# Kernel optimization log

Hardware: AMD Instinct MI355X
Metric: run time of the kernel (lower is better)

The kernel has to match this reference:

```python
import jax, jax.numpy as jnp
import numpy as np

NUM_Q = 4        # len(n_e_list)
N_E = 2048       # codes per quantizer level
E_DIM = 128      # e_dim
N_TOK = 32768    # flattened tokens
BETA = 0.25      # commitment coefficient


def setup_inputs() -> dict:
    key = jax.random.key(0)
    k_x, k_cb = jax.random.split(key)
    x = jax.random.normal(k_x, (N_TOK, E_DIM), dtype=jnp.float32)
    codebooks = jax.random.normal(k_cb, (NUM_Q, N_E, E_DIM), dtype=jnp.float32) * 0.1
    return {"x": x, "codebooks": codebooks, "use_freq": 0}


def _vq_layer(res, cb):
    # res: [N, D], cb: [K, D]
    # squared euclidean distance via expansion: ||r||^2 - 2 r.c + ||c||^2
    d = (jnp.sum(res * res, axis=-1, keepdims=True)
         - 2.0 * (res @ cb.T)
         + jnp.sum(cb * cb, axis=-1))            # [N, K]
    idx = jnp.argmin(d, axis=-1)                  # [N]
    q = cb[idx]                                   # [N, D] gather
    sg = jax.lax.stop_gradient
    # VQ-VAE loss: codebook term + beta * commitment term
    loss = jnp.mean((q - sg(res)) ** 2) + BETA * jnp.mean((sg(q) - res) ** 2)
    q_st = res + sg(q - res)                      # straight-through estimator
    return q_st, loss, idx


def reference(x, codebooks, use_freq):
    # residual chain over NUM_Q quantizer levels (sequential dependency)
    def step(carry, cb):
        residual, x_q = carry
        q, loss, idx = _vq_layer(residual, cb)
        return (residual - q, x_q + q), (loss, idx)

    (residual, x_q), (losses, indices) = jax.lax.scan(
        step, (x, jnp.zeros_like(x)), codebooks)
    mean_loss = jnp.mean(losses)
    all_indices = jnp.moveaxis(indices, 0, -1)    # [N, NUM_Q]
    return x_q, mean_loss, all_indices
```

## Files before the change

### kernel.cpp

```cpp
#include <hip/hip_runtime.h>

#define NTOK 32768
#define NE   2048
#define EDIM 128
#define NQ   4

#define TOKT 64
#define CHCODES 64
#define NCHUNK (NE / CHCODES)
#define CAP 16
#define MARGIN 0.25f

typedef __attribute__((ext_vector_type(8))) short short8v;
typedef __attribute__((ext_vector_type(4))) float f32x4;

__device__ __forceinline__ unsigned short bf16rne(float x) {
    unsigned u = __float_as_uint(x);
    unsigned r = 0x7FFFu + ((u >> 16) & 1u);
    return (unsigned short)((u + r) >> 16);
}

__device__ __forceinline__ void gld16(const void* g, const void* l) {
    __builtin_amdgcn_global_load_lds(
        (const __attribute__((address_space(1))) unsigned int*)g,
        (__attribute__((address_space(3))) unsigned int*)l, 16, 0, 0);
}

#define MFMA_BF16 __builtin_amdgcn_mfma_f32_16x16x32_bf16

__global__ __launch_bounds__(256) void prep_kernel(
    const float* __restrict__ cb, unsigned short* __restrict__ cb16s,
    float* __restrict__ cnorm, float* __restrict__ loss_accum)
{
    const int row = blockIdx.x * 256 + threadIdx.x;
    if (row == 0) *loss_accum = 0.0f;
    const float* src = cb + (size_t)row * EDIM;
    unsigned short* dst = cb16s + (size_t)row * EDIM;
    const int swz8 = (row & 7) << 3;
    float s = 0.0f;
#pragma unroll
    for (int j = 0; j < EDIM / 4; ++j) {
        float4 v = ((const float4*)src)[j];
        s += v.x * v.x; s += v.y * v.y; s += v.z * v.z; s += v.w * v.w;
        ushort4 o;
        o.x = bf16rne(v.x); o.y = bf16rne(v.y);
        o.z = bf16rne(v.z); o.w = bf16rne(v.w);
        *(ushort4*)(dst + ((j * 4) ^ swz8)) = o;
    }
    cnorm[row] = s;
}

__global__ __launch_bounds__(256, 2) void vq_level_kernel(
    const float* __restrict__ rin,
    const float* __restrict__ cbF,
    const unsigned short* __restrict__ cbL,
    const float* __restrict__ cnorm,
    float* __restrict__ rout,
    float* __restrict__ xq,
    float* __restrict__ idx_out,
    float* __restrict__ loss_accum,
    int level, int first)
{
    __shared__ __align__(16) float Af[TOKT][132];
    __shared__ __align__(16) unsigned short Bs[2][CHCODES * EDIM];
    __shared__ float part[4 * TOKT];
    __shared__ float rns[TOKT];
    __shared__ float mdw[2][TOKT];
    __shared__ int   cnt[TOKT];
    __shared__ int   lst[TOKT * CAP];
    __shared__ float redb_d[4][TOKT];
    __shared__ int   redb_i[4][TOKT];
    __shared__ int   idx_s[TOKT];
    __shared__ float lsum[256];

    const int t     = threadIdx.x;
    const int tok0  = blockIdx.x * TOKT;
    const int w     = t >> 6;
    const int rh    = w >> 1;
    const int chalf = w & 1;
    const int cl    = t & 15;
    const int lg    = (t & 63) >> 4;
    if (t < TOKT) cnt[t] = 0;

    {
        const int tok = t & 63;
        const int dg  = t >> 6;
        float s = 0.0f;
#pragma unroll
        for (int j = 0; j < 8; ++j) {
            const int d0 = dg * 32 + j * 4;
            float4 v = *(const float4*)(rin + (size_t)(tok0 + tok) * EDIM + d0);
            *(float4*)&Af[tok][d0] = v;
            s += v.x * v.x; s += v.y * v.y; s += v.z * v.z; s += v.w * v.w;
        }
        part[dg * TOKT + tok] = s;
    }
    __syncthreads();
    if (t < TOKT)
        rns[t] = ((part[t] + part[TOKT + t]) + part[2 * TOKT + t])
                 + part[3 * TOKT + t];

    short8v a00, a01, a02, a03, a10, a11, a12, a13;
#define LDA(AF, AROW, KT) { \
    float4 p0 = *(const float4*)&Af[AROW][(KT) * 32 + lg * 8]; \
    float4 p1 = *(const float4*)&Af[AROW][(KT) * 32 + lg * 8 + 4]; \
    AF[0] = (short)bf16rne(p0.x); AF[1] = (short)bf16rne(p0.y); \
    AF[2] = (short)bf16rne(p0.z); AF[3] = (short)bf16rne(p0.w); \
    AF[4] = (short)bf16rne(p1.x); AF[5] = (short)bf16rne(p1.y); \
    AF[6] = (short)bf16rne(p1.z); AF[7] = (short)bf16rne(p1.w); }
    {
        const int ar0 = rh * 32 + cl, ar1 = rh * 32 + 16 + cl;
        LDA(a00, ar0, 0) LDA(a01, ar0, 1) LDA(a02, ar0, 2) LDA(a03, ar0, 3)
        LDA(a10, ar1, 0) LDA(a11, ar1, 1) LDA(a12, ar1, 2) LDA(a13, ar1, 3)
    }
#undef LDA

    const int swzk = (cl & 7) << 4;
    const int inn0 = (0   + lg * 16) ^ swzk;
    const int inn1 = (64  + lg * 16) ^ swzk;
    const int inn2 = (128 + lg * 16) ^ swzk;
    const int inn3 = (192 + lg * 16) ^ swzk;

#define STAGE(DST, CH) { \
    const char* gs = (const char*)cbL + (size_t)(CH) * 16384 + t * 16; \
    char* ls = (char*)(DST) + (t & 192) * 16; \
    gld16(gs,         ls); \
    gld16(gs + 4096,  ls + 4096); \
    gld16(gs + 8192,  ls + 8192); \
    gld16(gs + 12288, ls + 12288); }

#define MFMAG(BUFC, CH, CT, TAIL) { \
    const char* bp = (const char*)&Bs[BUFC][0] \
                     + (chalf * 32 + (CT) * 16 + cl) * 256; \
    short8v b0 = *(const short8v*)(bp + inn0); \
    short8v b1 = *(const short8v*)(bp + inn1); \
    short8v b2 = *(const short8v*)(bp + inn2); \
    short8v b3 = *(const short8v*)(bp + inn3); \
    f32x4 ac0 = {0.f, 0.f, 0.f, 0.f}; \
    f32x4 ac1 = {0.f, 0.f, 0.f, 0.f}; \
    ac0 = MFMA_BF16(a00, b0, ac0, 0, 0, 0); \
    ac0 = MFMA_BF16(a01, b1, ac0, 0, 0, 0); \
    ac0 = MFMA_BF16(a02, b2, ac0, 0, 0, 0); \
    ac0 = MFMA_BF16(a03, b3, ac0, 0, 0, 0); \
    ac1 = MFMA_BF16(a10, b0, ac1, 0, 0, 0); \
    ac1 = MFMA_BF16(a11, b1, ac1, 0, 0, 0); \
    ac1 = MFMA_BF16(a12, b2, ac1, 0, 0, 0); \
    ac1 = MFMA_BF16(a13, b3, ac1, 0, 0, 0); \
    const int code = (CH) * CHCODES + chalf * 32 + (CT) * 16 + cl; \
    const float cn = cnorm[code]; \
    TAIL }

#define T_MIN \
    md00 = fminf(md00, (rn00 - 2.f * ac0[0]) + cn); \
    md01 = fminf(md01, (rn01 - 2.f * ac0[1]) + cn); \
    md02 = fminf(md02, (rn02 - 2.f * ac0[2]) + cn); \
    md03 = fminf(md03, (rn03 - 2.f * ac0[3]) + cn); \
    md10 = fminf(md10, (rn10 - 2.f * ac1[0]) + cn); \
    md11 = fminf(md11, (rn11 - 2.f * ac1[1]) + cn); \
    md12 = fminf(md12, (rn12 - 2.f * ac1[2]) + cn); \
    md13 = fminf(md13, (rn13 - 2.f * ac1[3]) + cn);

#define PUSH(AC, R, RN, TH, TOKB) { \
    float dd = ((RN) - 2.f * AC[R]) + cn; \
    if (dd < (TH)) { int p = atomicAdd(&cnt[(TOKB) + R], 1); \
                     if (p < CAP) lst[((TOKB) + R) * CAP + p] = code; } }
#define T_CAND \
    PUSH(ac0, 0, rn00, th00, tokb0) PUSH(ac0, 1, rn01, th01, tokb0) \
    PUSH(ac0, 2, rn02, th02, tokb0) PUSH(ac0, 3, rn03, th03, tokb0) \
    PUSH(ac1, 0, rn10, th10, tokb1) PUSH(ac1, 1, rn11, th11, tokb1) \
    PUSH(ac1, 2, rn12, th12, tokb1) PUSH(ac1, 3, rn13, th13, tokb1)

#define CH_P1(B, CH) { MFMAG(B, CH, 0, T_MIN)  MFMAG(B, CH, 1, T_MIN)  }
#define CH_P2(B, CH) { MFMAG(B, CH, 0, T_CAND) MFMAG(B, CH, 1, T_CAND) }

    STAGE(&Bs[0][0], 0)
    __syncthreads();

    const int tokb0 = rh * 32 + lg * 4;
    const int tokb1 = tokb0 + 16;
    const float rn00 = rns[tokb0 + 0], rn01 = rns[tokb0 + 1];
    const float rn02 = rns[tokb0 + 2], rn03 = rns[tokb0 + 3];
    const float rn10 = rns[tokb1 + 0], rn11 = rns[tokb1 + 1];
    const float rn12 = rns[tokb1 + 2], rn13 = rns[tokb1 + 3];

    float md00 = 3.402823466e38f, md01 = md00, md02 = md00, md03 = md00;
    float md10 = md00, md11 = md00, md12 = md00, md13 = md00;

    for (int c2 = 0; c2 < NCHUNK / 2; ++c2) {
        const int c = c2 * 2;
        STAGE(&Bs[1][0], c + 1)
        CH_P1(0, c)
        __syncthreads();
        if (c + 2 < NCHUNK) STAGE(&Bs[0][0], c + 2)
        CH_P1(1, c + 1)
        __syncthreads();
    }

#pragma unroll
    for (int m = 1; m < 16; m <<= 1) {
        md00 = fminf(md00, __shfl_xor(md00, m, 64));
        md01 = fminf(md01, __shfl_xor(md01, m, 64));
        md02 = fminf(md02, __shfl_xor(md02, m, 64));
        md03 = fminf(md03, __shfl_xor(md03, m, 64));
        md10 = fminf(md10, __shfl_xor(md10, m, 64));
        md11 = fminf(md11, __shfl_xor(md11, m, 64));
        md12 = fminf(md12, __shfl_xor(md12, m, 64));
        md13 = fminf(md13, __shfl_xor(md13, m, 64));
    }
    if (cl == 0) {
        mdw[chalf][tokb0 + 0] = md00; mdw[chalf][tokb0 + 1] = md01;
        mdw[chalf][tokb0 + 2] = md02; mdw[chalf][tokb0 + 3] = md03;
        mdw[chalf][tokb1 + 0] = md10; mdw[chalf][tokb1 + 1] = md11;
        mdw[chalf][tokb1 + 2] = md12; mdw[chalf][tokb1 + 3] = md13;
    }

    STAGE(&Bs[0][0], 0)
    __syncthreads();

    const float th00 = fminf(mdw[0][tokb0 + 0], mdw[1][tokb0 + 0]) + MARGIN;
    const float th01 = fminf(mdw[0][tokb0 + 1], mdw[1][tokb0 + 1]) + MARGIN;
    const float th02 = fminf(mdw[0][tokb0 + 2], mdw[1][tokb0 + 2]) + MARGIN;
    const float th03 = fminf(mdw[0][tokb0 + 3], mdw[1][tokb0 + 3]) + MARGIN;
    const float th10 = fminf(mdw[0][tokb1 + 0], mdw[1][tokb1 + 0]) + MARGIN;
    const float th11 = fminf(mdw[0][tokb1 + 1], mdw[1][tokb1 + 1]) + MARGIN;
    const float th12 = fminf(mdw[0][tokb1 + 2], mdw[1][tokb1 + 2]) + MARGIN;
    const float th13 = fminf(mdw[0][tokb1 + 3], mdw[1][tokb1 + 3]) + MARGIN;

    for (int c2 = 0; c2 < NCHUNK / 2; ++c2) {
        const int c = c2 * 2;
        STAGE(&Bs[1][0], c + 1)
        CH_P2(0, c)
        __syncthreads();
        if (c + 2 < NCHUNK) STAGE(&Bs[0][0], c + 2)
        CH_P2(1, c + 1)
        __syncthreads();
    }

    {
        const int tok = t & 63;
        const int s   = t >> 6;
        const int n   = min(cnt[tok], CAP);
        const float rn_t = rns[tok];
        float bd = 3.402823466e38f;
        int   bi = 0x7fffffff;
        for (int i = s; i < n; i += 4) {
            const int c = lst[tok * CAP + i];
            const float* cr = cbF + (size_t)c * EDIM;
            float dot = 0.0f;
#pragma unroll 8
            for (int d = 0; d < EDIM; ++d)
                dot = fmaf(Af[tok][d], cr[d], dot);
            const float dd = (rn_t - 2.0f * dot) + cnorm[c];
            if (dd < bd || (dd == bd && c < bi)) { bd = dd; bi = c; }
        }
        redb_d[s][tok] = bd;
        redb_i[s][tok] = bi;
    }
    __syncthreads();
    if (t < TOKT) {
        float bd = redb_d[0][t];
        int   bi = redb_i[0][t];
#pragma unroll
        for (int s = 1; s < 4; ++s) {
            const float dd = redb_d[s][t];
            const int   ii = redb_i[s][t];
            if (dd < bd || (dd == bd && ii < bi)) { bd = dd; bi = ii; }
        }
        idx_s[t] = bi;
        idx_out[(size_t)(tok0 + t) * NQ + level] = (float)bi;
    }
    __syncthreads();

    {
        const int tok = t >> 2;
        const int dq  = t & 3;
        const int gi  = idx_s[tok];
        const float* qrow = cbF + (size_t)gi * EDIM;
        float lp = 0.0f;
#pragma unroll
        for (int k = 0; k < 8; ++k) {
            const int d0 = k * 16 + dq * 4;
            const float4 q = *(const float4*)(qrow + d0);
            const float4 r = *(const float4*)&Af[tok][d0];
            float4 tq, qst, rnv;
            tq.x = q.x - r.x; tq.y = q.y - r.y; tq.z = q.z - r.z; tq.w = q.w - r.w;
            qst.x = r.x + tq.x; qst.y = r.y + tq.y;
            qst.z = r.z + tq.z; qst.w = r.w + tq.w;
            rnv.x = r.x - qst.x; rnv.y = r.y - qst.y;
            rnv.z = r.z - qst.z; rnv.w = r.w - qst.w;
            const size_t go = (size_t)(tok0 + tok) * EDIM + d0;
            *(float4*)(rout + go) = rnv;
            if (first) {
                *(float4*)(xq + go) = qst;
            } else {
                float4 o = *(const float4*)(xq + go);
                o.x += qst.x; o.y += qst.y; o.z += qst.z; o.w += qst.w;
                *(float4*)(xq + go) = o;
            }
            lp += tq.x * tq.x; lp += tq.y * tq.y;
            lp += tq.z * tq.z; lp += tq.w * tq.w;
        }
        lsum[t] = lp;
    }
    __syncthreads();
#pragma unroll
    for (int s2 = 128; s2 > 0; s2 >>= 1) {
        if (t < s2) lsum[t] += lsum[t + s2];
        __syncthreads();
    }
    if (t == 0) atomicAdd(loss_accum, lsum[0]);
}

__global__ void finalize_kernel(const float* __restrict__ loss_accum,
                                float* __restrict__ out_loss)
{
    *out_loss = *loss_accum * (1.25f / (4.0f * (float)NTOK * (float)EDIM));
}

extern "C" void kernel_launch(void* const* d_in, const int* in_sizes, int n_in,
                              void* d_out, int out_size, void* d_ws, size_t ws_size,
                              hipStream_t stream)
{
    const float* x  = (const float*)d_in[0];
    const float* cb = (const float*)d_in[1];

    float* out      = (float*)d_out;
    float* xq       = out;
    float* out_loss = out + (size_t)NTOK * EDIM;
    float* idx_out  = out + (size_t)NTOK * EDIM + 1;

    float* ws             = (float*)d_ws;
    float* cnorm          = ws;
    float* loss_accum     = ws + 8192;
    unsigned short* cb16s = (unsigned short*)(ws + 8448);
    float* r0             = ws + 8448 + (size_t)NQ * NE * EDIM / 2;

    prep_kernel<<<(NQ * NE) / 256, 256, 0, stream>>>(cb, cb16s, cnorm, loss_accum);

    for (int l = 0; l < NQ; ++l) {
        const float* rin = (l == 0) ? x : r0;
        vq_level_kernel<<<NTOK / TOKT, 256, 0, stream>>>(
            rin, cb + (size_t)l * NE * EDIM,
            cb16s + (size_t)l * NE * EDIM,
            cnorm + (size_t)l * NE,
            r0, xq, idx_out, loss_accum, l, (l == 0) ? 1 : 0);
    }
    finalize_kernel<<<1, 1, 0, stream>>>(loss_accum, out_loss);
}
```

Baseline: 291.7 us.

## Replace two-pass bf16 argmin with single pass plus per-half-chunk max filtering

Removes the second full MFMA sweep over the codebook. A single pass now computes scores (dot minus half the code norm, folded into the accumulator init), keeps a per-token running max, and records a ceiling-encoded 16-bit max for each 32-code half-chunk in shared memory. Half-chunks whose max lies within a margin of the best are placed on a worklist and rescored exactly in fp32, with a packed 64-bit atomicMin picking the winner. This halves MFMA and LDS staging work and drops the per-code atomic candidate pushes, at the cost of rescoring 32 codes per surviving half-chunk, a worklist cap of 512 that can overflow and drop candidates, and shared buffers aliased onto the staging buffer.

```diff
diff --git a/kernel.cpp b/kernel.cpp
--- a/kernel.cpp
+++ b/kernel.cpp
@@ -8,8 +8,9 @@
 #define TOKT 64
 #define CHCODES 64
 #define NCHUNK (NE / CHCODES)
-#define CAP 16
-#define MARGIN 0.25f
+#define NHC 64
+#define WLCAP 512
+#define MARGIN_S 0.25f
 
 typedef __attribute__((ext_vector_type(8))) short short8v;
 typedef __attribute__((ext_vector_type(4))) float f32x4;
@@ -18,6 +19,14 @@
     unsigned u = __float_as_uint(x);
     unsigned r = 0x7FFFu + ((u >> 16) & 1u);
     return (unsigned short)((u + r) >> 16);
+}
+
+__device__ __forceinline__ unsigned enc32f(float f) {
+    unsigned u = __float_as_uint(f);
+    return u ^ ((unsigned)((int)u >> 31) | 0x80000000u);
+}
+__device__ __forceinline__ unsigned short enc16ceil(float f) {
+    return (unsigned short)((enc32f(f) >> 16) + 1);
 }
 
 __device__ __forceinline__ void gld16(const void* g, const void* l) {
@@ -63,15 +72,18 @@
 {
     __shared__ __align__(16) float Af[TOKT][132];
     __shared__ __align__(16) unsigned short Bs[2][CHCODES * EDIM];
-    __shared__ float part[4 * TOKT];
+    __shared__ unsigned short chm[TOKT * NHC];
     __shared__ float rns[TOKT];
-    __shared__ float mdw[2][TOKT];
-    __shared__ int   cnt[TOKT];
-    __shared__ int   lst[TOKT * CAP];
-    __shared__ float redb_d[4][TOKT];
-    __shared__ int   redb_i[4][TOKT];
-    __shared__ int   idx_s[TOKT];
-    __shared__ float lsum[256];
+
+    float* part = (float*)&Bs[1][0];
+    char*  ov   = (char*)&Bs[0][0];
+    unsigned long long* best = (unsigned long long*)ov;
+    int*   wl    = (int*)(ov + 512);
+    int*   wcnt  = (int*)(ov + 2560);
+    float* smaxs = (float*)(ov + 2576);
+    float* mdw   = (float*)(ov + 2832);
+    int*   idx_s = (int*)(ov + 3344);
+    float* lsum  = (float*)(ov + 3600);
 
     const int t     = threadIdx.x;
     const int tok0  = blockIdx.x * TOKT;
@@ -80,7 +92,6 @@
     const int chalf = w & 1;
     const int cl    = t & 15;
     const int lg    = (t & 63) >> 4;
-    if (t < TOKT) cnt[t] = 0;
 
     {
         const int tok = t & 63;
@@ -129,143 +140,171 @@
     gld16(gs + 8192,  ls + 8192); \
     gld16(gs + 12288, ls + 12288); }
 
-#define MFMAG(BUFC, CH, CT, TAIL) { \
-    const char* bp = (const char*)&Bs[BUFC][0] \
-                     + (chalf * 32 + (CT) * 16 + cl) * 256; \
-    short8v b0 = *(const short8v*)(bp + inn0); \
-    short8v b1 = *(const short8v*)(bp + inn1); \
-    short8v b2 = *(const short8v*)(bp + inn2); \
-    short8v b3 = *(const short8v*)(bp + inn3); \
-    f32x4 ac0 = {0.f, 0.f, 0.f, 0.f}; \
-    f32x4 ac1 = {0.f, 0.f, 0.f, 0.f}; \
-    ac0 = MFMA_BF16(a00, b0, ac0, 0, 0, 0); \
-    ac0 = MFMA_BF16(a01, b1, ac0, 0, 0, 0); \
-    ac0 = MFMA_BF16(a02, b2, ac0, 0, 0, 0); \
-    ac0 = MFMA_BF16(a03, b3, ac0, 0, 0, 0); \
-    ac1 = MFMA_BF16(a10, b0, ac1, 0, 0, 0); \
-    ac1 = MFMA_BF16(a11, b1, ac1, 0, 0, 0); \
-    ac1 = MFMA_BF16(a12, b2, ac1, 0, 0, 0); \
-    ac1 = MFMA_BF16(a13, b3, ac1, 0, 0, 0); \
-    const int code = (CH) * CHCODES + chalf * 32 + (CT) * 16 + cl; \
-    const float cn = cnorm[code]; \
-    TAIL }
-
-#define T_MIN \
-    md00 = fminf(md00, (rn00 - 2.f * ac0[0]) + cn); \
-    md01 = fminf(md01, (rn01 - 2.f * ac0[1]) + cn); \
-    md02 = fminf(md02, (rn02 - 2.f * ac0[2]) + cn); \
-    md03 = fminf(md03, (rn03 - 2.f * ac0[3]) + cn); \
-    md10 = fminf(md10, (rn10 - 2.f * ac1[0]) + cn); \
-    md11 = fminf(md11, (rn11 - 2.f * ac1[1]) + cn); \
-    md12 = fminf(md12, (rn12 - 2.f * ac1[2]) + cn); \
-    md13 = fminf(md13, (rn13 - 2.f * ac1[3]) + cn);
-
-#define PUSH(AC, R, RN, TH, TOKB) { \
-    float dd = ((RN) - 2.f * AC[R]) + cn; \
-    if (dd < (TH)) { int p = atomicAdd(&cnt[(TOKB) + R], 1); \
-                     if (p < CAP) lst[((TOKB) + R) * CAP + p] = code; } }
-#define T_CAND \
-    PUSH(ac0, 0, rn00, th00, tokb0) PUSH(ac0, 1, rn01, th01, tokb0) \
-    PUSH(ac0, 2, rn02, th02, tokb0) PUSH(ac0, 3, rn03, th03, tokb0) \
-    PUSH(ac1, 0, rn10, th10, tokb1) PUSH(ac1, 1, rn11, th11, tokb1) \
-    PUSH(ac1, 2, rn12, th12, tokb1) PUSH(ac1, 3, rn13, th13, tokb1)
-
-#define CH_P1(B, CH) { MFMAG(B, CH, 0, T_MIN)  MFMAG(B, CH, 1, T_MIN)  }
-#define CH_P2(B, CH) { MFMAG(B, CH, 0, T_CAND) MFMAG(B, CH, 1, T_CAND) }
-
-    STAGE(&Bs[0][0], 0)
-    __syncthreads();
-
     const int tokb0 = rh * 32 + lg * 4;
     const int tokb1 = tokb0 + 16;
-    const float rn00 = rns[tokb0 + 0], rn01 = rns[tokb0 + 1];
-    const float rn02 = rns[tokb0 + 2], rn03 = rns[tokb0 + 3];
-    const float rn10 = rns[tokb1 + 0], rn11 = rns[tokb1 + 1];
-    const float rn12 = rns[tokb1 + 2], rn13 = rns[tokb1 + 3];
-
-    float md00 = 3.402823466e38f, md01 = md00, md02 = md00, md03 = md00;
+
+#define CHUNK(BUFC, CH) { \
+    const char* bpA = (const char*)&Bs[BUFC][0] + (chalf * 32 + cl) * 256; \
+    const int codeA = (CH) * 64 + chalf * 32 + cl; \
+    const float cnA = -0.5f * cnorm[codeA]; \
+    const float cnB = -0.5f * cnorm[codeA + 16]; \
+    short8v b0 = *(const short8v*)(bpA + inn0); \
+    short8v b1 = *(const short8v*)(bpA + inn1); \
+    short8v b2 = *(const short8v*)(bpA + inn2); \
+    short8v b3 = *(const short8v*)(bpA + inn3); \
+    f32x4 p00 = {cnA, cnA, cnA, cnA}; \
+    f32x4 p01 = {cnA, cnA, cnA, cnA}; \
+    p00 = MFMA_BF16(a00, b0, p00, 0, 0, 0); \
+    p00 = MFMA_BF16(a01, b1, p00, 0, 0, 0); \
+    p00 = MFMA_BF16(a02, b2, p00, 0, 0, 0); \
+    p00 = MFMA_BF16(a03, b3, p00, 0, 0, 0); \
+    p01 = MFMA_BF16(a10, b0, p01, 0, 0, 0); \
+    p01 = MFMA_BF16(a11, b1, p01, 0, 0, 0); \
+    p01 = MFMA_BF16(a12, b2, p01, 0, 0, 0); \
+    p01 = MFMA_BF16(a13, b3, p01, 0, 0, 0); \
+    const char* bpB = bpA + 16 * 256; \
+    b0 = *(const short8v*)(bpB + inn0); \
+    b1 = *(const short8v*)(bpB + inn1); \
+    b2 = *(const short8v*)(bpB + inn2); \
+    b3 = *(const short8v*)(bpB + inn3); \
+    f32x4 p10 = {cnB, cnB, cnB, cnB}; \
+    f32x4 p11 = {cnB, cnB, cnB, cnB}; \
+    p10 = MFMA_BF16(a00, b0, p10, 0, 0, 0); \
+    p10 = MFMA_BF16(a01, b1, p10, 0, 0, 0); \
+    p10 = MFMA_BF16(a02, b2, p10, 0, 0, 0); \
+    p10 = MFMA_BF16(a03, b3, p10, 0, 0, 0); \
+    p11 = MFMA_BF16(a10, b0, p11, 0, 0, 0); \
+    p11 = MFMA_BF16(a11, b1, p11, 0, 0, 0); \
+    p11 = MFMA_BF16(a12, b2, p11, 0, 0, 0); \
+    p11 = MFMA_BF16(a13, b3, p11, 0, 0, 0); \
+    float lm0 = fmaxf(p00[0], p10[0]); md00 = fmaxf(md00, lm0); \
+    float lm1 = fmaxf(p00[1], p10[1]); md01 = fmaxf(md01, lm1); \
+    float lm2 = fmaxf(p00[2], p10[2]); md02 = fmaxf(md02, lm2); \
+    float lm3 = fmaxf(p00[3], p10[3]); md03 = fmaxf(md03, lm3); \
+    float lm4 = fmaxf(p01[0], p11[0]); md10 = fmaxf(md10, lm4); \
+    float lm5 = fmaxf(p01[1], p11[1]); md11 = fmaxf(md11, lm5); \
+    float lm6 = fmaxf(p01[2], p11[2]); md12 = fmaxf(md12, lm6); \
+    float lm7 = fmaxf(p01[3], p11[3]); md13 = fmaxf(md13, lm7); \
+    _Pragma("unroll") \
+    for (int m = 1; m < 16; m <<= 1) { \
+        lm0 = fmaxf(lm0, __shfl_xor(lm0, m, 64)); \
+        lm1 = fmaxf(lm1, __shfl_xor(lm1, m, 64)); \
+        lm2 = fmaxf(lm2, __shfl_xor(lm2, m, 64)); \
+        lm3 = fmaxf(lm3, __shfl_xor(lm3, m, 64)); \
+        lm4 = fmaxf(lm4, __shfl_xor(lm4, m, 64)); \
+        lm5 = fmaxf(lm5, __shfl_xor(lm5, m, 64)); \
+        lm6 = fmaxf(lm6, __shfl_xor(lm6, m, 64)); \
+        lm7 = fmaxf(lm7, __shfl_xor(lm7, m, 64)); \
+    } \
+    if (cl == 0) { \
+        const int hc = (CH) * 2 + chalf; \
+        chm[(tokb0 + 0) * NHC + hc] = enc16ceil(lm0); \
+        chm[(tokb0 + 1) * NHC + hc] = enc16ceil(lm1); \
+        chm[(tokb0 + 2) * NHC + hc] = enc16ceil(lm2); \
+        chm[(tokb0 + 3) * NHC + hc] = enc16ceil(lm3); \
+        chm[(tokb1 + 0) * NHC + hc] = enc16ceil(lm4); \
+        chm[(tokb1 + 1) * NHC + hc] = enc16ceil(lm5); \
+        chm[(tokb1 + 2) * NHC + hc] = enc16ceil(lm6); \
+        chm[(tokb1 + 3) * NHC + hc] = enc16ceil(lm7); \
+    } }
+
+    STAGE(&Bs[0][0], 0)
+    __syncthreads();
+
+    float md00 = -3.402823466e38f, md01 = md00, md02 = md00, md03 = md00;
     float md10 = md00, md11 = md00, md12 = md00, md13 = md00;
 
     for (int c2 = 0; c2 < NCHUNK / 2; ++c2) {
         const int c = c2 * 2;
         STAGE(&Bs[1][0], c + 1)
-        CH_P1(0, c)
+        CHUNK(0, c)
         __syncthreads();
         if (c + 2 < NCHUNK) STAGE(&Bs[0][0], c + 2)
-        CH_P1(1, c + 1)
+        CHUNK(1, c + 1)
         __syncthreads();
     }
+#undef CHUNK
 
 #pragma unroll
     for (int m = 1; m < 16; m <<= 1) {
-        md00 = fminf(md00, __shfl_xor(md00, m, 64));
-        md01 = fminf(md01, __shfl_xor(md01, m, 64));
-        md02 = fminf(md02, __shfl_xor(md02, m, 64));
-        md03 = fminf(md03, __shfl_xor(md03, m, 64));
-        md10 = fminf(md10, __shfl_xor(md10, m, 64));
-        md11 = fminf(md11, __shfl_xor(md11, m, 64));
-        md12 = fminf(md12, __shfl_xor(md12, m, 64));
-        md13 = fminf(md13, __shfl_xor(md13, m, 64));
+        md00 = fmaxf(md00, __shfl_xor(md00, m, 64));
+        md01 = fmaxf(md01, __shfl_xor(md01, m, 64));
+        md02 = fmaxf(md02, __shfl_xor(md02, m, 64));
+        md03 = fmaxf(md03, __shfl_xor(md03, m, 64));
+        md10 = fmaxf(md10, __shfl_xor(md10, m, 64));
+        md11 = fmaxf(md11, __shfl_xor(md11, m, 64));
+        md12 = fmaxf(md12, __shfl_xor(md12, m, 64));
+        md13 = fmaxf(md13, __shfl_xor(md13, m, 64));
     }
     if (cl == 0) {
-        mdw[chalf][tokb0 + 0] = md00; mdw[chalf][tokb0 + 1] = md01;
-        mdw[chalf][tokb0 + 2] = md02; mdw[chalf][tokb0 + 3] = md03;
-        mdw[chalf][tokb1 + 0] = md10; mdw[chalf][tokb1 + 1] = md11;
-        mdw[chalf][tokb1 + 2] = md12; mdw[chalf][tokb1 + 3] = md13;
-    }
-
-    STAGE(&Bs[0][0], 0)
-    __syncthreads();
-
-    const float th00 = fminf(mdw[0][tokb0 + 0], mdw[1][tokb0 + 0]) + MARGIN;
-    const float th01 = fminf(mdw[0][tokb0 + 1], mdw[1][tokb0 + 1]) + MARGIN;
-    const float th02 = fminf(mdw[0][tokb0 + 2], mdw[1][tokb0 + 2]) + MARGIN;
-    const float th03 = fminf(mdw[0][tokb0 + 3], mdw[1][tokb0 + 3]) + MARGIN;
-    const float th10 = fminf(mdw[0][tokb1 + 0], mdw[1][tokb1 + 0]) + MARGIN;
-    const float th11 = fminf(mdw[0][tokb1 + 1], mdw[1][tokb1 + 1]) + MARGIN;
-    const float th12 = fminf(mdw[0][tokb1 + 2], mdw[1][tokb1 + 2]) + MARGIN;
-    const float th13 = fminf(mdw[0][tokb1 + 3], mdw[1][tokb1 + 3]) + MARGIN;
-
-    for (int c2 = 0; c2 < NCHUNK / 2; ++c2) {
-        const int c = c2 * 2;
-        STAGE(&Bs[1][0], c + 1)
-        CH_P2(0, c)
-        __syncthreads();
-        if (c + 2 < NCHUNK) STAGE(&Bs[0][0], c + 2)
-        CH_P2(1, c + 1)
-        __syncthreads();
-    }
-
-    {
-        const int tok = t & 63;
-        const int s   = t >> 6;
-        const int n   = min(cnt[tok], CAP);
-        const float rn_t = rns[tok];
-        float bd = 3.402823466e38f;
-        int   bi = 0x7fffffff;
-        for (int i = s; i < n; i += 4) {
-            const int c = lst[tok * CAP + i];
-            const float* cr = cbF + (size_t)c * EDIM;
-            float dot = 0.0f;
-#pragma unroll 8
-            for (int d = 0; d < EDIM; ++d)
-                dot = fmaf(Af[tok][d], cr[d], dot);
-            const float dd = (rn_t - 2.0f * dot) + cnorm[c];
-            if (dd < bd || (dd == bd && c < bi)) { bd = dd; bi = c; }
+        mdw[chalf * TOKT + tokb0 + 0] = md00;
+        mdw[chalf * TOKT + tokb0 + 1] = md01;
+        mdw[chalf * TOKT + tokb0 + 2] = md02;
+        mdw[chalf * TOKT + tokb0 + 3] = md03;
+        mdw[chalf * TOKT + tokb1 + 0] = md10;
+        mdw[chalf * TOKT + tokb1 + 1] = md11;
+        mdw[chalf * TOKT + tokb1 + 2] = md12;
+        mdw[chalf * TOKT + tokb1 + 3] = md13;
+    }
+    __syncthreads();
+
+    if (t < TOKT) {
+        smaxs[t] = fmaxf(mdw[t], mdw[TOKT + t]);
+        best[t]  = 0xFFFFFFFFFFFFFFFFULL;
+    }
+    if (t == 0) *wcnt = 0;
+    __syncthreads();
+
+    {
+        const int tok = t >> 2;
+        const unsigned short th16 =
+            (unsigned short)(enc32f(smaxs[tok] - MARGIN_S) >> 16);
+        const int hbase = (t & 3) * 16;
+#pragma unroll
+        for (int k = 0; k < 16; ++k) {
+            const int hc = hbase + k;
+            if (chm[tok * NHC + hc] >= th16) {
+                const int p = atomicAdd(wcnt, 1);
+                if (p < WLCAP) wl[p] = (hc << 6) | tok;
+            }
         }
-        redb_d[s][tok] = bd;
-        redb_i[s][tok] = bi;
-    }
-    __syncthreads();
+    }
+    __syncthreads();
+
+    {
+        const int n   = min(*wcnt, WLCAP);
+        const int sub = t & 3;
+        for (int it = t >> 2; it < n; it += 64) {
+            const int e   = wl[it];
+            const int tok = e & 63;
+            const int hc  = e >> 6;
+            const float rn_t = rns[tok];
+            float bd = 3.402823466e38f;
+            int   bi = 0x7fffffff;
+#pragma unroll
+            for (int k = 0; k < 8; ++k) {
+                const int code = hc * 32 + sub + k * 4;
+                const float* cr = cbF + (size_t)code * EDIM;
+                float dot = 0.0f;
+#pragma unroll
+                for (int j = 0; j < 32; ++j) {
+                    const float4 a = *(const float4*)&Af[tok][j * 4];
+                    const float4 b = *(const float4*)(cr + j * 4);
+                    dot = fmaf(a.x, b.x, dot); dot = fmaf(a.y, b.y, dot);
+                    dot = fmaf(a.z, b.z, dot); dot = fmaf(a.w, b.w, dot);
+                }
+                const float dd = (rn_t - 2.0f * dot) + cnorm[code];
+                if (dd < bd || (dd == bd && code < bi)) { bd = dd; bi = code; }
+            }
+            const unsigned long long pk =
+                ((unsigned long long)enc32f(bd) << 32) | (unsigned)bi;
+            atomicMin(&best[tok], pk);
+        }
+    }
+    __syncthreads();
+
     if (t < TOKT) {
-        float bd = redb_d[0][t];
-        int   bi = redb_i[0][t];
-#pragma unroll
-        for (int s = 1; s < 4; ++s) {
-            const float dd = redb_d[s][t];
-            const int   ii = redb_i[s][t];
-            if (dd < bd || (dd == bd && ii < bi)) { bd = dd; bi = ii; }
-        }
+        const int bi = (int)(best[t] & 0xFFFFFFFFu);
         idx_s[t] = bi;
         idx_out[(size_t)(tok0 + t) * NQ + level] = (float)bi;
     }
```

After: 889.0 us. 205% more time.

## Retile VQ distance search: each wave covers all 64 tokens, score folded into MFMA

Applied to the files above, without the earlier changes.

Each wave now holds A fragments for all 64 tokens and a 32-code slice of a 128-code chunk, so every B fragment loaded from LDS feeds four MFMAs instead of two. The score is rewritten as r·c − ½‖c‖², with −½‖c‖² used as the MFMA accumulator init and a max-reduction replacing the min, which drops the per-element rn/cn arithmetic. The candidate margin is rescaled to match. The fp32 residual LDS tile is removed and the rescoring and epilogue read the residual from global memory instead. This raises register pressure (16 A fragments plus 16 running maxima) and doubles the B staging buffer, which may reduce occupancy under launch_bounds(256,2).

```diff
diff --git a/kernel.cpp b/kernel.cpp
--- a/kernel.cpp
+++ b/kernel.cpp
@@ -6,10 +6,10 @@
 #define NQ   4
 
 #define TOKT 64
-#define CHCODES 64
+#define CHCODES 128
 #define NCHUNK (NE / CHCODES)
 #define CAP 16
-#define MARGIN 0.25f
+#define MARGIN_S 0.1875f
 
 typedef __attribute__((ext_vector_type(8))) short short8v;
 typedef __attribute__((ext_vector_type(4))) float f32x4;
@@ -61,11 +61,11 @@
     float* __restrict__ loss_accum,
     int level, int first)
 {
-    __shared__ __align__(16) float Af[TOKT][132];
     __shared__ __align__(16) unsigned short Bs[2][CHCODES * EDIM];
     __shared__ float part[4 * TOKT];
     __shared__ float rns[TOKT];
-    __shared__ float mdw[2][TOKT];
+    __shared__ float mdw[4][TOKT];
+    __shared__ float smaxs[TOKT];
     __shared__ int   cnt[TOKT];
     __shared__ int   lst[TOKT * CAP];
     __shared__ float redb_d[4][TOKT];
@@ -73,13 +73,11 @@
     __shared__ int   idx_s[TOKT];
     __shared__ float lsum[256];
 
-    const int t     = threadIdx.x;
-    const int tok0  = blockIdx.x * TOKT;
-    const int w     = t >> 6;
-    const int rh    = w >> 1;
-    const int chalf = w & 1;
-    const int cl    = t & 15;
-    const int lg    = (t & 63) >> 4;
+    const int t    = threadIdx.x;
+    const int tok0 = blockIdx.x * TOKT;
+    const int w    = t >> 6;
+    const int cl   = t & 15;
+    const int lg   = (t & 63) >> 4;
     if (t < TOKT) cnt[t] = 0;
 
     {
@@ -90,7 +88,6 @@
         for (int j = 0; j < 8; ++j) {
             const int d0 = dg * 32 + j * 4;
             float4 v = *(const float4*)(rin + (size_t)(tok0 + tok) * EDIM + d0);
-            *(float4*)&Af[tok][d0] = v;
             s += v.x * v.x; s += v.y * v.y; s += v.z * v.z; s += v.w * v.w;
         }
         part[dg * TOKT + tok] = s;
@@ -101,18 +98,19 @@
                  + part[3 * TOKT + t];
 
     short8v a00, a01, a02, a03, a10, a11, a12, a13;
-#define LDA(AF, AROW, KT) { \
-    float4 p0 = *(const float4*)&Af[AROW][(KT) * 32 + lg * 8]; \
-    float4 p1 = *(const float4*)&Af[AROW][(KT) * 32 + lg * 8 + 4]; \
-    AF[0] = (short)bf16rne(p0.x); AF[1] = (short)bf16rne(p0.y); \
-    AF[2] = (short)bf16rne(p0.z); AF[3] = (short)bf16rne(p0.w); \
-    AF[4] = (short)bf16rne(p1.x); AF[5] = (short)bf16rne(p1.y); \
-    AF[6] = (short)bf16rne(p1.z); AF[7] = (short)bf16rne(p1.w); }
-    {
-        const int ar0 = rh * 32 + cl, ar1 = rh * 32 + 16 + cl;
-        LDA(a00, ar0, 0) LDA(a01, ar0, 1) LDA(a02, ar0, 2) LDA(a03, ar0, 3)
-        LDA(a10, ar1, 0) LDA(a11, ar1, 1) LDA(a12, ar1, 2) LDA(a13, ar1, 3)
-    }
+    short8v a20, a21, a22, a23, a30, a31, a32, a33;
+#define LDA(AF, RT, KT) { \
+    const float* ap = rin + (size_t)(tok0 + (RT) * 16 + cl) * EDIM \
+                      + (KT) * 32 + lg * 8; \
+    float4 q0 = *(const float4*)ap; float4 q1 = *(const float4*)(ap + 4); \
+    AF[0] = (short)bf16rne(q0.x); AF[1] = (short)bf16rne(q0.y); \
+    AF[2] = (short)bf16rne(q0.z); AF[3] = (short)bf16rne(q0.w); \
+    AF[4] = (short)bf16rne(q1.x); AF[5] = (short)bf16rne(q1.y); \
+    AF[6] = (short)bf16rne(q1.z); AF[7] = (short)bf16rne(q1.w); }
+    LDA(a00, 0, 0) LDA(a01, 0, 1) LDA(a02, 0, 2) LDA(a03, 0, 3)
+    LDA(a10, 1, 0) LDA(a11, 1, 1) LDA(a12, 1, 2) LDA(a13, 1, 3)
+    LDA(a20, 2, 0) LDA(a21, 2, 1) LDA(a22, 2, 2) LDA(a23, 2, 3)
+    LDA(a30, 3, 0) LDA(a31, 3, 1) LDA(a32, 3, 2) LDA(a33, 3, 3)
 #undef LDA
 
     const int swzk = (cl & 7) << 4;
@@ -121,70 +119,75 @@
     const int inn2 = (128 + lg * 16) ^ swzk;
     const int inn3 = (192 + lg * 16) ^ swzk;
 
+    const int tb0 = lg * 4, tb1 = 16 + lg * 4, tb2 = 32 + lg * 4, tb3 = 48 + lg * 4;
+
 #define STAGE(DST, CH) { \
-    const char* gs = (const char*)cbL + (size_t)(CH) * 16384 + t * 16; \
+    const char* gs = (const char*)cbL + (size_t)(CH) * 32768 + t * 16; \
     char* ls = (char*)(DST) + (t & 192) * 16; \
-    gld16(gs,         ls); \
-    gld16(gs + 4096,  ls + 4096); \
-    gld16(gs + 8192,  ls + 8192); \
-    gld16(gs + 12288, ls + 12288); }
-
-#define MFMAG(BUFC, CH, CT, TAIL) { \
+    gld16(gs,          ls); \
+    gld16(gs + 4096,   ls + 4096); \
+    gld16(gs + 8192,   ls + 8192); \
+    gld16(gs + 12288,  ls + 12288); \
+    gld16(gs + 16384,  ls + 16384); \
+    gld16(gs + 20480,  ls + 20480); \
+    gld16(gs + 24576,  ls + 24576); \
+    gld16(gs + 28672,  ls + 28672); }
+
+#define CTBLK(BUFC, CH, CT, TAIL) { \
+    const int code = (CH) * CHCODES + w * 32 + (CT) * 16 + cl; \
+    const float cn2 = -0.5f * cnorm[code]; \
     const char* bp = (const char*)&Bs[BUFC][0] \
-                     + (chalf * 32 + (CT) * 16 + cl) * 256; \
-    short8v b0 = *(const short8v*)(bp + inn0); \
-    short8v b1 = *(const short8v*)(bp + inn1); \
-    short8v b2 = *(const short8v*)(bp + inn2); \
-    short8v b3 = *(const short8v*)(bp + inn3); \
-    f32x4 ac0 = {0.f, 0.f, 0.f, 0.f}; \
-    f32x4 ac1 = {0.f, 0.f, 0.f, 0.f}; \
-    ac0 = MFMA_BF16(a00, b0, ac0, 0, 0, 0); \
-    ac0 = MFMA_BF16(a01, b1, ac0, 0, 0, 0); \
-    ac0 = MFMA_BF16(a02, b2, ac0, 0, 0, 0); \
-    ac0 = MFMA_BF16(a03, b3, ac0, 0, 0, 0); \
-    ac1 = MFMA_BF16(a10, b0, ac1, 0, 0, 0); \
-    ac1 = MFMA_BF16(a11, b1, ac1, 0, 0, 0); \
-    ac1 = MFMA_BF16(a12, b2, ac1, 0, 0, 0); \
-    ac1 = MFMA_BF16(a13, b3, ac1, 0, 0, 0); \
-    const int code = (CH) * CHCODES + chalf * 32 + (CT) * 16 + cl; \
-    const float cn = cnorm[code]; \
+                     + (w * 32 + (CT) * 16 + cl) * 256; \
+    f32x4 p0 = {cn2, cn2, cn2, cn2}; f32x4 p1 = p0; \
+    f32x4 p2 = p0;                   f32x4 p3 = p0; \
+    short8v bb; \
+    bb = *(const short8v*)(bp + inn0); \
+    p0 = MFMA_BF16(a00, bb, p0, 0, 0, 0); p1 = MFMA_BF16(a10, bb, p1, 0, 0, 0); \
+    p2 = MFMA_BF16(a20, bb, p2, 0, 0, 0); p3 = MFMA_BF16(a30, bb, p3, 0, 0, 0); \
+    bb = *(const short8v*)(bp + inn1); \
+    p0 = MFMA_BF16(a01, bb, p0, 0, 0, 0); p1 = MFMA_BF16(a11, bb, p1, 0, 0, 0); \
+    p2 = MFMA_BF16(a21, bb, p2, 0, 0, 0); p3 = MFMA_BF16(a31, bb, p3, 0, 0, 0); \
+    bb = *(const short8v*)(bp + inn2); \
+    p0 = MFMA_BF16(a02, bb, p0, 0, 0, 0); p1 = MFMA_BF16(a12, bb, p1, 0, 0, 0); \
+    p2 = MFMA_BF16(a22, bb, p2, 0, 0, 0); p3 = MFMA_BF16(a32, bb, p3, 0, 0, 0); \
+    bb = *(const short8v*)(bp + inn3); \
+    p0 = MFMA_BF16(a03, bb, p0, 0, 0, 0); p1 = MFMA_BF16(a13, bb, p1, 0, 0, 0); \
+    p2 = MFMA_BF16(a23, bb, p2, 0, 0, 0); p3 = MFMA_BF16(a33, bb, p3, 0, 0, 0); \
     TAIL }
 
 #define T_MIN \
-    md00 = fminf(md00, (rn00 - 2.f * ac0[0]) + cn); \
-    md01 = fminf(md01, (rn01 - 2.f * ac0[1]) + cn); \
-    md02 = fminf(md02, (rn02 - 2.f * ac0[2]) + cn); \
-    md03 = fminf(md03, (rn03 - 2.f * ac0[3]) + cn); \
-    md10 = fminf(md10, (rn10 - 2.f * ac1[0]) + cn); \
-    md11 = fminf(md11, (rn11 - 2.f * ac1[1]) + cn); \
-    md12 = fminf(md12, (rn12 - 2.f * ac1[2]) + cn); \
-    md13 = fminf(md13, (rn13 - 2.f * ac1[3]) + cn);
-
-#define PUSH(AC, R, RN, TH, TOKB) { \
-    float dd = ((RN) - 2.f * AC[R]) + cn; \
-    if (dd < (TH)) { int p = atomicAdd(&cnt[(TOKB) + R], 1); \
-                     if (p < CAP) lst[((TOKB) + R) * CAP + p] = code; } }
-#define T_CAND \
-    PUSH(ac0, 0, rn00, th00, tokb0) PUSH(ac0, 1, rn01, th01, tokb0) \
-    PUSH(ac0, 2, rn02, th02, tokb0) PUSH(ac0, 3, rn03, th03, tokb0) \
-    PUSH(ac1, 0, rn10, th10, tokb1) PUSH(ac1, 1, rn11, th11, tokb1) \
-    PUSH(ac1, 2, rn12, th12, tokb1) PUSH(ac1, 3, rn13, th13, tokb1)
-
-#define CH_P1(B, CH) { MFMAG(B, CH, 0, T_MIN)  MFMAG(B, CH, 1, T_MIN)  }
-#define CH_P2(B, CH) { MFMAG(B, CH, 0, T_CAND) MFMAG(B, CH, 1, T_CAND) }
+    md00 = fmaxf(md00, p0[0]); md01 = fmaxf(md01, p0[1]); \
+    md02 = fmaxf(md02, p0[2]); md03 = fmaxf(md03, p0[3]); \
+    md10 = fmaxf(md10, p1[0]); md11 = fmaxf(md11, p1[1]); \
+    md12 = fmaxf(md12, p1[2]); md13 = fmaxf(md13, p1[3]); \
+    md20 = fmaxf(md20, p2[0]); md21 = fmaxf(md21, p2[1]); \
+    md22 = fmaxf(md22, p2[2]); md23 = fmaxf(md23, p2[3]); \
+    md30 = fmaxf(md30, p3[0]); md31 = fmaxf(md31, p3[1]); \
+    md32 = fmaxf(md32, p3[2]); md33 = fmaxf(md33, p3[3]);
+
+#define PUSH1(S, TH, TOK) { if ((S) > (TH)) { \
+    int pp = atomicAdd(&cnt[TOK], 1); \
+    if (pp < CAP) lst[(TOK) * CAP + pp] = code; } }
+#define T_PUSH \
+    PUSH1(p0[0], th00, tb0 + 0) PUSH1(p0[1], th01, tb0 + 1) \
+    PUSH1(p0[2], th02, tb0 + 2) PUSH1(p0[3], th03, tb0 + 3) \
+    PUSH1(p1[0], th10, tb1 + 0) PUSH1(p1[1], th11, tb1 + 1) \
+    PUSH1(p1[2], th12, tb1 + 2) PUSH1(p1[3], th13, tb1 + 3) \
+    PUSH1(p2[0], th20, tb2 + 0) PUSH1(p2[1], th21, tb2 + 1) \
+    PUSH1(p2[2], th22, tb2 + 2) PUSH1(p2[3], th23, tb2 + 3) \
+    PUSH1(p3[0], th30, tb3 + 0) PUSH1(p3[1], th31, tb3 + 1) \
+    PUSH1(p3[2], th32, tb3 + 2) PUSH1(p3[3], th33, tb3 + 3)
+
+#define CH_P1(B, CH) { CTBLK(B, CH, 0, T_MIN)  CTBLK(B, CH, 1, T_MIN)  }
+#define CH_P2(B, CH) { CTBLK(B, CH, 0, T_PUSH) CTBLK(B, CH, 1, T_PUSH) }
 
     STAGE(&Bs[0][0], 0)
     __syncthreads();
 
-    const int tokb0 = rh * 32 + lg * 4;
-    const int tokb1 = tokb0 + 16;
-    const float rn00 = rns[tokb0 + 0], rn01 = rns[tokb0 + 1];
-    const float rn02 = rns[tokb0 + 2], rn03 = rns[tokb0 + 3];
-    const float rn10 = rns[tokb1 + 0], rn11 = rns[tokb1 + 1];
-    const float rn12 = rns[tokb1 + 2], rn13 = rns[tokb1 + 3];
-
-    float md00 = 3.402823466e38f, md01 = md00, md02 = md00, md03 = md00;
+    float md00 = -3.402823466e38f, md01 = md00, md02 = md00, md03 = md00;
     float md10 = md00, md11 = md00, md12 = md00, md13 = md00;
+    float md20 = md00, md21 = md00, md22 = md00, md23 = md00;
+    float md30 = md00, md31 = md00, md32 = md00, md33 = md00;
 
     for (int c2 = 0; c2 < NCHUNK / 2; ++c2) {
         const int c = c2 * 2;
@@ -196,35 +199,59 @@
         __syncthreads();
     }
 
+    STAGE(&Bs[0][0], 0)
+
 #pragma unroll
     for (int m = 1; m < 16; m <<= 1) {
-        md00 = fminf(md00, __shfl_xor(md00, m, 64));
-        md01 = fminf(md01, __shfl_xor(md01, m, 64));
-        md02 = fminf(md02, __shfl_xor(md02, m, 64));
-        md03 = fminf(md03, __shfl_xor(md03, m, 64));
-        md10 = fminf(md10, __shfl_xor(md10, m, 64));
-        md11 = fminf(md11, __shfl_xor(md11, m, 64));
-        md12 = fminf(md12, __shfl_xor(md12, m, 64));
-        md13 = fminf(md13, __shfl_xor(md13, m, 64));
+        md00 = fmaxf(md00, __shfl_xor(md00, m, 64));
+        md01 = fmaxf(md01, __shfl_xor(md01, m, 64));
+        md02 = fmaxf(md02, __shfl_xor(md02, m, 64));
+        md03 = fmaxf(md03, __shfl_xor(md03, m, 64));
+        md10 = fmaxf(md10, __shfl_xor(md10, m, 64));
+        md11 = fmaxf(md11, __shfl_xor(md11, m, 64));
+        md12 = fmaxf(md12, __shfl_xor(md12, m, 64));
+        md13 = fmaxf(md13, __shfl_xor(md13, m, 64));
+        md20 = fmaxf(md20, __shfl_xor(md20, m, 64));
+        md21 = fmaxf(md21, __shfl_xor(md21, m, 64));
+        md22 = fmaxf(md22, __shfl_xor(md22, m, 64));
+        md23 = fmaxf(md23, __shfl_xor(md23, m, 64));
+        md30 = fmaxf(md30, __shfl_xor(md30, m, 64));
+        md31 = fmaxf(md31, __shfl_xor(md31, m, 64));
+        md32 = fmaxf(md32, __shfl_xor(md32, m, 64));
+        md33 = fmaxf(md33, __shfl_xor(md33, m, 64));
     }
     if (cl == 0) {
-        mdw[chalf][tokb0 + 0] = md00; mdw[chalf][tokb0 + 1] = md01;
-        mdw[chalf][tokb0 + 2] = md02; mdw[chalf][tokb0 + 3] = md03;
-        mdw[chalf][tokb1 + 0] = md10; mdw[chalf][tokb1 + 1] = md11;
-        mdw[chalf][tokb1 + 2] = md12; mdw[chalf][tokb1 + 3] = md13;
-    }
-
-    STAGE(&Bs[0][0], 0)
-    __syncthreads();
-
-    const float th00 = fminf(mdw[0][tokb0 + 0], mdw[1][tokb0 + 0]) + MARGIN;
-    const float th01 = fminf(mdw[0][tokb0 + 1], mdw[1][tokb0 + 1]) + MARGIN;
-    const float th02 = fminf(mdw[0][tokb0 + 2], mdw[1][tokb0 + 2]) + MARGIN;
-    const float th03 = fminf(mdw[0][tokb0 + 3], mdw[1][tokb0 + 3]) + MARGIN;
-    const float th10 = fminf(mdw[0][tokb1 + 0], mdw[1][tokb1 + 0]) + MARGIN;
-    const float th11 = fminf(mdw[0][tokb1 + 1], mdw[1][tokb1 + 1]) + MARGIN;
-    const float th12 = fminf(mdw[0][tokb1 + 2], mdw[1][tokb1 + 2]) + MARGIN;
-    const float th13 = fminf(mdw[0][tokb1 + 3], mdw[1][tokb1 + 3]) + MARGIN;
+        mdw[w][tb0 + 0] = md00; mdw[w][tb0 + 1] = md01;
+        mdw[w][tb0 + 2] = md02; mdw[w][tb0 + 3] = md03;
+        mdw[w][tb1 + 0] = md10; mdw[w][tb1 + 1] = md11;
+        mdw[w][tb1 + 2] = md12; mdw[w][tb1 + 3] = md13;
+        mdw[w][tb2 + 0] = md20; mdw[w][tb2 + 1] = md21;
+        mdw[w][tb2 + 2] = md22; mdw[w][tb2 + 3] = md23;
+        mdw[w][tb3 + 0] = md30; mdw[w][tb3 + 1] = md31;
+        mdw[w][tb3 + 2] = md32; mdw[w][tb3 + 3] = md33;
+    }
+    __syncthreads();
+    if (t < TOKT)
+        smaxs[t] = fmaxf(fmaxf(mdw[0][t], mdw[1][t]),
+                         fmaxf(mdw[2][t], mdw[3][t]));
+    __syncthreads();
+
+    const float th00 = smaxs[tb0 + 0] - MARGIN_S;
+    const float th01 = smaxs[tb0 + 1] - MARGIN_S;
+    const float th02 = smaxs[tb0 + 2] - MARGIN_S;
+    const float th03 = smaxs[tb0 + 3] - MARGIN_S;
+    const float th10 = smaxs[tb1 + 0] - MARGIN_S;
+    const float th11 = smaxs[tb1 + 1] - MARGIN_S;
+    const float th12 = smaxs[tb1 + 2] - MARGIN_S;
+    const float th13 = smaxs[tb1 + 3] - MARGIN_S;
+    const float th20 = smaxs[tb2 + 0] - MARGIN_S;
+    const float th21 = smaxs[tb2 + 1] - MARGIN_S;
+    const float th22 = smaxs[tb2 + 2] - MARGIN_S;
+    const float th23 = smaxs[tb2 + 3] - MARGIN_S;
+    const float th30 = smaxs[tb3 + 0] - MARGIN_S;
+    const float th31 = smaxs[tb3 + 1] - MARGIN_S;
+    const float th32 = smaxs[tb3 + 2] - MARGIN_S;
+    const float th33 = smaxs[tb3 + 3] - MARGIN_S;
 
     for (int c2 = 0; c2 < NCHUNK / 2; ++c2) {
         const int c = c2 * 2;
@@ -241,15 +268,20 @@
         const int s   = t >> 6;
         const int n   = min(cnt[tok], CAP);
         const float rn_t = rns[tok];
+        const float* rrow = rin + (size_t)(tok0 + tok) * EDIM;
         float bd = 3.402823466e38f;
         int   bi = 0x7fffffff;
         for (int i = s; i < n; i += 4) {
             const int c = lst[tok * CAP + i];
             const float* cr = cbF + (size_t)c * EDIM;
             float dot = 0.0f;
-#pragma unroll 8
-            for (int d = 0; d < EDIM; ++d)
-                dot = fmaf(Af[tok][d], cr[d], dot);
+#pragma unroll
+            for (int j = 0; j < 32; ++j) {
+                const float4 a = *(const float4*)(rrow + j * 4);
+                const float4 b = *(const float4*)(cr + j * 4);
+                dot = fmaf(a.x, b.x, dot); dot = fmaf(a.y, b.y, dot);
+                dot = fmaf(a.z, b.z, dot); dot = fmaf(a.w, b.w, dot);
+            }
             const float dd = (rn_t - 2.0f * dot) + cnorm[c];
             if (dd < bd || (dd == bd && c < bi)) { bd = dd; bi = c; }
         }
@@ -276,12 +308,13 @@
         const int dq  = t & 3;
         const int gi  = idx_s[tok];
         const float* qrow = cbF + (size_t)gi * EDIM;
+        const float* rrow = rin + (size_t)(tok0 + tok) * EDIM;
         float lp = 0.0f;
 #pragma unroll
         for (int k = 0; k < 8; ++k) {
             const int d0 = k * 16 + dq * 4;
             const float4 q = *(const float4*)(qrow + d0);
-            const float4 r = *(const float4*)&Af[tok][d0];
+            const float4 r = *(const float4*)(rrow + d0);
             float4 tq, qst, rnv;
             tq.x = q.x - r.x; tq.y = q.y - r.y; tq.z = q.z - r.z; tq.w = q.w - r.w;
             qst.x = r.x + tq.x; qst.y = r.y + tq.y;
```

New measurement: 313.7 us. 7.6% more time.
